# Performance work log

Measured on AMD Instinct MI355X. Metric: run time of the kernel, lower is better.

Reference implementation:

```python
import jax, jax.numpy as jnp
import numpy as np

CLAMP = 80.0


def setup_inputs() -> dict:
    key = jax.random.key(0)
    ks = jax.random.split(key, 8)
    B, C, D, H, W = 2, 64, 16, 16, 16
    Ck = C // 8  # qk channel dim
    x = jax.random.normal(ks[0], (B, C, D, H, W), dtype=jnp.float32)
    # 1x1x1 Conv3d == pointwise linear over channels
    wq = jax.random.normal(ks[1], (Ck, C), dtype=jnp.float32) * (1.0 / np.sqrt(C))
    bq = jnp.zeros((Ck,), dtype=jnp.float32)
    wk = jax.random.normal(ks[2], (Ck, C), dtype=jnp.float32) * (1.0 / np.sqrt(C))
    bk = jnp.zeros((Ck,), dtype=jnp.float32)
    wv = jax.random.normal(ks[3], (C, C), dtype=jnp.float32) * (1.0 / np.sqrt(C))
    bv = jnp.zeros((C,), dtype=jnp.float32)
    gamma = jnp.zeros((1,), dtype=jnp.float32)
    return {"x": x, "wq": wq, "bq": bq, "wk": wk, "bk": bk,
            "wv": wv, "bv": bv, "gamma": gamma}


def reference(x, wq, bq, wk, bk, wv, bv, gamma):
    B, C, D, H, W = x.shape
    N = D * H * W
    scale = 1.0 / np.sqrt(max(C // 8, 1))
    xf = x.reshape(B, C, N)
    # 1x1 convs as channel matmuls -> [B, Cq, N] / [B, C, N]
    q = jnp.einsum('oc,bcn->bon', wq, xf) + bq[None, :, None]
    k = jnp.einsum('oc,bcn->bon', wk, xf) + bk[None, :, None]
    v = jnp.einsum('oc,bcn->bon', wv, xf) + bv[None, :, None]
    q32, k32, v32 = q.astype(jnp.float32), k.astype(jnp.float32), v.astype(jnp.float32)
    # logits[b,n,m] = sum_o q[b,o,n] k[b,o,m] * scale  (q^T k)
    logits = jnp.einsum('bon,bom->bnm', q32, k32) * scale
    logits = jnp.clip(logits, -CLAMP, CLAMP)
    attn = jax.nn.softmax(logits, axis=-1)  # rows sum to 1
    # out = v @ attn  (note: attn applied on the right, as in source)
    out32 = jnp.einsum('bcn,bnm->bcm', v32, attn)
    out = out32.reshape(B, C, D, H, W).astype(x.dtype)
    return gamma[0] * out + x
```

## Files before the change

kernel.cpp:

```cpp
#include <hip/hip_runtime.h>

#define S2F (0.35355339059327373f * 1.4426950408889634f)

using h2 = decltype(__builtin_amdgcn_cvt_pkrtz(0.0f, 0.0f));
typedef _Float16 half8 __attribute__((ext_vector_type(8)));
typedef float f32x4 __attribute__((ext_vector_type(4)));

static __device__ __forceinline__ h2 u2h(unsigned u) { return __builtin_bit_cast(h2, u); }
static __device__ __forceinline__ unsigned pkf16(float a, float b) {
  return __builtin_bit_cast(unsigned, __builtin_amdgcn_cvt_pkrtz(a, b));
}
static __device__ __forceinline__ half8 u4h8(uint4 u) { return __builtin_bit_cast(half8, u); }


__global__ void __launch_bounds__(256, 4)
qkv_kernel(const float* __restrict__ x,
           const float* __restrict__ wq, const float* __restrict__ bq,
           const float* __restrict__ wk, const float* __restrict__ bk,
           const float* __restrict__ wv, const float* __restrict__ bv,
           unsigned* __restrict__ q4, unsigned* __restrict__ k4,
           unsigned* __restrict__ v16) {
  __shared__ float wls[16][64];
  __shared__ float bias16[16];
  __shared__ float qk_lds[16][32];
  int t = threadIdx.x;
  int bid = blockIdx.x;
  int b = bid / 640;
  int rem = bid - b * 640;
  int tile = rem / 5;
  int type = rem - tile * 5;
  int n0 = tile << 5;
  int j = t & 31, rg = t >> 5;

  float* wflat = &wls[0][0];
  for (int i = t; i < 1024; i += 256) {
    float wv_;
    if (type == 0) wv_ = (i < 512) ? wq[i] : wk[i - 512];
    else           wv_ = wv[((type - 1) << 10) + i];
    wflat[i] = wv_;
  }
  if (t < 16)
    bias16[t] = (type == 0) ? ((t < 8) ? bq[t] : bk[t - 8])
                            : bv[((type - 1) << 4) + t];
  __syncthreads();

  float res0 = bias16[rg * 2], res1 = bias16[rg * 2 + 1];
  const float* xb = x + ((b * 64) << 12) + n0 + j;
  #pragma unroll 1
  for (int c0 = 0; c0 < 64; c0 += 16) {
    float xr[16];
    #pragma unroll
    for (int cc = 0; cc < 16; ++cc) xr[cc] = xb[(c0 + cc) << 12];
    const float4* w0 = (const float4*)&wls[rg * 2][c0];
    const float4* w1 = (const float4*)&wls[rg * 2 + 1][c0];
    #pragma unroll
    for (int c4 = 0; c4 < 4; ++c4) {
      float4 a = w0[c4], bb = w1[c4];
      res0 += a.x * xr[4*c4] + a.y * xr[4*c4+1] + a.z * xr[4*c4+2] + a.w * xr[4*c4+3];
      res1 += bb.x * xr[4*c4] + bb.y * xr[4*c4+1] + bb.z * xr[4*c4+2] + bb.w * xr[4*c4+3];
    }
  }

  if (type == 0) {
    qk_lds[rg * 2][j] = res0;
    qk_lds[rg * 2 + 1][j] = res1;
    __syncthreads();
    if (t < 64) {
      int jj = t & 31;
      bool isq = t < 32;
      int rb = isq ? 0 : 8;
      float sc = isq ? S2F : 1.0f;
      uint4 u;
      u.x = pkf16(sc * qk_lds[rb + 0][jj], sc * qk_lds[rb + 1][jj]);
      u.y = pkf16(sc * qk_lds[rb + 2][jj], sc * qk_lds[rb + 3][jj]);
      u.z = pkf16(sc * qk_lds[rb + 4][jj], sc * qk_lds[rb + 5][jj]);
      u.w = pkf16(sc * qk_lds[rb + 6][jj], sc * qk_lds[rb + 7][jj]);
      unsigned* dst = isq ? q4 : k4;
      *(uint4*)&dst[((b << 12) + n0 + jj) << 2] = u;
    }
  } else {
    int cbase = (type - 1) << 4;
    unsigned nb0 = (unsigned)__builtin_amdgcn_ds_swizzle(
        __builtin_bit_cast(int, res0), 0x041F);
    unsigned nb1 = (unsigned)__builtin_amdgcn_ds_swizzle(
        __builtin_bit_cast(int, res1), 0x041F);
    if (!(j & 1)) {
      int half = (n0 >> 1) + (j >> 1);
      v16[(((b << 6) + cbase + rg * 2) << 11) + half]     = pkf16(res0, __builtin_bit_cast(float, nb0));
      v16[(((b << 6) + cbase + rg * 2 + 1) << 11) + half] = pkf16(res1, __builtin_bit_cast(float, nb1));
    }
  }
}

__global__ void __launch_bounds__(256, 4)
rowsum_kernel(const unsigned* __restrict__ q4, const unsigned* __restrict__ k4,
              float* __restrict__ lsv2) {
  __shared__ float ps[8][33];
  int t = threadIdx.x;
  int b = blockIdx.x >> 9;
  int nt0 = (blockIdx.x & 511) << 3;
  int tn = t & 7, tg = t >> 3;
  uint4 qu = *(const uint4*)&q4[((b << 12) + nt0 + tn) << 2];
  h2 q0 = u2h(qu.x), q1 = u2h(qu.y), q2 = u2h(qu.z), q3 = u2h(qu.w);
  float acc = 0.f;
  int m0 = tg << 7;
  #pragma unroll 4
  for (int m = m0; m < m0 + 128; ++m) {
    uint4 ka = *(const uint4*)&k4[((b << 12) + m) << 2];
    float l = __builtin_amdgcn_fdot2(u2h(ka.x), q0, 0.f, false);
    l = __builtin_amdgcn_fdot2(u2h(ka.y), q1, l, false);
    l = __builtin_amdgcn_fdot2(u2h(ka.z), q2, l, false);
    l = __builtin_amdgcn_fdot2(u2h(ka.w), q3, l, false);
    acc += exp2f(l);
  }
  ps[tn][tg] = acc;
  __syncthreads();
  if (t < 8) {
    float s = 0.f;
    #pragma unroll
    for (int j = 0; j < 32; ++j) s += ps[t][j];
    lsv2[(b << 12) + nt0 + t] = -__log2f(s);
  }
}

__global__ void __launch_bounds__(512, 1)
attnout_kernel(const float* __restrict__ x, const unsigned* __restrict__ q4,
               const unsigned* __restrict__ k4, const unsigned* __restrict__ v16,
               const float* __restrict__ lsv2, const float* __restrict__ gamma,
               float* __restrict__ out) {
  __shared__ float red[8][64][36];
  int t = threadIdx.x;
  int b = blockIdx.x >> 7;
  int m0 = (blockIdx.x & 127) << 5;
  int w = t >> 6, l = t & 63;
  int L15 = l & 15, G = l >> 4;
  int permG = ((G & 1) << 1) | (G >> 1);
  bool even = (G & 1) == 0;

  uint4 bk2[2];
  #pragma unroll
  for (int mh = 0; mh < 2; ++mh) {
    if (l < 16) bk2[mh] = *(const uint4*)&k4[((b << 12) + m0 + mh * 16 + L15) << 2];
    else        bk2[mh] = make_uint4(0, 0, 0, 0);
  }
  f32x4 acc[2][4];
  #pragma unroll
  for (int mh = 0; mh < 2; ++mh)
    #pragma unroll
    for (int cf = 0; cf < 4; ++cf) acc[mh][cf] = (f32x4){0.f, 0.f, 0.f, 0.f};

  const float* svb = lsv2 + (b << 12);
  const unsigned* q4b = q4 + ((long)(b << 12) << 2);
  const unsigned* v16b = v16 + ((long)(b << 6) << 11);

  auto LOAD = [&](int step, half8& aq0, half8& aq1, f32x4& sv0, f32x4& sv1,
                  uint4* va) {
    int n0 = (w << 9) + (step << 5);
    aq0 = u4h8(*(const uint4*)&q4b[(n0 + L15) << 2]);
    aq1 = u4h8(*(const uint4*)&q4b[(n0 + 16 + L15) << 2]);
    sv0 = *(const f32x4*)&svb[n0 + (G << 2)];
    sv1 = *(const f32x4*)&svb[n0 + 16 + (G << 2)];
    #pragma unroll
    for (int cf = 0; cf < 4; ++cf)
      va[cf] = *(const uint4*)&v16b[(((cf << 4) + L15) << 11) + (n0 >> 1) + (permG << 2)];
  };
  auto COMPUTE = [&](half8 aq0, half8 aq1, f32x4 sv0, f32x4 sv1, const uint4* va) {
    #pragma unroll
    for (int mh = 0; mh < 2; ++mh) {
      f32x4 z = {0.f, 0.f, 0.f, 0.f};
      f32x4 d0 = __builtin_amdgcn_mfma_f32_16x16x32_f16(aq0, u4h8(bk2[mh]), z, 0, 0, 0);
      f32x4 d1 = __builtin_amdgcn_mfma_f32_16x16x32_f16(aq1, u4h8(bk2[mh]), z, 0, 0, 0);
      float p0[4], p1[4];
      #pragma unroll
      for (int r = 0; r < 4; ++r) {
        p0[r] = exp2f(d0[r] + sv0[r]);
        p1[r] = exp2f(d1[r] + sv1[r]);
      }
      unsigned x0 = pkf16(p0[0], p0[1]), x1 = pkf16(p0[2], p0[3]);
      unsigned y0 = pkf16(p1[0], p1[1]), y1 = pkf16(p1[2], p1[3]);
      unsigned snd0 = even ? y0 : x0;
      unsigned snd1 = even ? y1 : x1;
      unsigned r0 = (unsigned)__builtin_amdgcn_ds_swizzle((int)snd0, 0x401F);
      unsigned r1 = (unsigned)__builtin_amdgcn_ds_swizzle((int)snd1, 0x401F);
      uint4 Bu;
      Bu.x = even ? x0 : r0;
      Bu.y = even ? x1 : r1;
      Bu.z = even ? r0 : y0;
      Bu.w = even ? r1 : y1;
      half8 Bf = u4h8(Bu);
      #pragma unroll
      for (int cf = 0; cf < 4; ++cf)
        acc[mh][cf] = __builtin_amdgcn_mfma_f32_16x16x32_f16(u4h8(va[cf]), Bf, acc[mh][cf], 0, 0, 0);
    }
  };

  half8 aq0A, aq1A, aq0B, aq1B;
  f32x4 sv0A, sv1A, sv0B, sv1B;
  uint4 vaA[4], vaB[4];
  LOAD(0, aq0A, aq1A, sv0A, sv1A, vaA);
  #pragma unroll 1
  for (int step = 0; step < 16; step += 2) {
    LOAD(step + 1, aq0B, aq1B, sv0B, sv1B, vaB);
    COMPUTE(aq0A, aq1A, sv0A, sv1A, vaA);
    if (step < 14) LOAD(step + 2, aq0A, aq1A, sv0A, sv1A, vaA);
    COMPUTE(aq0B, aq1B, sv0B, sv1B, vaB);
  }

  #pragma unroll
  for (int mh = 0; mh < 2; ++mh)
    #pragma unroll
    for (int cf = 0; cf < 4; ++cf)
      *(f32x4*)&red[w][l][(mh * 4 + cf) * 4] = acc[mh][cf];
  __syncthreads();
  int rl = t & 63, f = t >> 6;
  float g = gamma[0];
  f32x4 s = {0.f, 0.f, 0.f, 0.f};
  #pragma unroll
  for (int ww = 0; ww < 8; ++ww) s += *(const f32x4*)&red[ww][rl][f * 4];
  int mh = f >> 2, cf = f & 3;
  int m = m0 + mh * 16 + (rl & 15);
  int cb = cf * 16 + ((rl >> 4) << 2);
  #pragma unroll
  for (int r = 0; r < 4; ++r) {
    int idx = (((b << 6) + cb + r) << 12) + m;
    out[idx] = g * s[r] + x[idx];
  }
}

extern "C" void kernel_launch(void* const* d_in, const int* in_sizes, int n_in,
                              void* d_out, int out_size, void* d_ws, size_t ws_size,
                              hipStream_t stream) {
  const float* x     = (const float*)d_in[0];
  const float* wq    = (const float*)d_in[1];
  const float* bq    = (const float*)d_in[2];
  const float* wk    = (const float*)d_in[3];
  const float* bk    = (const float*)d_in[4];
  const float* wv    = (const float*)d_in[5];
  const float* bv    = (const float*)d_in[6];
  const float* gamma = (const float*)d_in[7];
  float* out = (float*)d_out;
  unsigned* wsu = (unsigned*)d_ws;
  unsigned* q4  = wsu;
  unsigned* k4  = wsu + 32768;
  unsigned* v16 = wsu + 65536;
  float*    lsv2 = (float*)(wsu + 327680);

  qkv_kernel<<<1280, 256, 0, stream>>>(x, wq, bq, wk, bk, wv, bv, q4, k4, v16);
  rowsum_kernel<<<1024, 256, 0, stream>>>(q4, k4, lsv2);
  attnout_kernel<<<256, 512, 0, stream>>>(x, q4, k4, v16, lsv2, gamma, out);
}
```

Baseline: 49.75 us.

## Double attnout block to 16 waves splitting the key-row range across more warps

Raises attnout_kernel from 8 to 16 waves per block so each wave handles 256 instead of 512 of the n positions, doubling per-CU latency hiding for the MFMA/exp loop. Q and log-sum values are now loaded inside compute instead of being double-buffered, to save registers. The cross-wave reduction becomes two-stage (upper waves write, lower waves add), and the final write is split so each thread stores two rows. This adds an extra barrier and LDS pass, and 1024-thread blocks with a register cap could cause spills.

```diff
diff --git a/kernel.cpp b/kernel.cpp
--- a/kernel.cpp
+++ b/kernel.cpp
@@ -123,7 +123,7 @@
   }
 }
 
-__global__ void __launch_bounds__(512, 1)
+__global__ void __launch_bounds__(1024, 1)
 attnout_kernel(const float* __restrict__ x, const unsigned* __restrict__ q4,
                const unsigned* __restrict__ k4, const unsigned* __restrict__ v16,
                const float* __restrict__ lsv2, const float* __restrict__ gamma,
@@ -153,18 +153,18 @@
   const unsigned* q4b = q4 + ((long)(b << 12) << 2);
   const unsigned* v16b = v16 + ((long)(b << 6) << 11);
 
-  auto LOAD = [&](int step, half8& aq0, half8& aq1, f32x4& sv0, f32x4& sv1,
-                  uint4* va) {
-    int n0 = (w << 9) + (step << 5);
-    aq0 = u4h8(*(const uint4*)&q4b[(n0 + L15) << 2]);
-    aq1 = u4h8(*(const uint4*)&q4b[(n0 + 16 + L15) << 2]);
-    sv0 = *(const f32x4*)&svb[n0 + (G << 2)];
-    sv1 = *(const f32x4*)&svb[n0 + 16 + (G << 2)];
+  auto LOADVA = [&](int step, uint4* va) {
+    int n0 = (w << 8) + (step << 5);
     #pragma unroll
     for (int cf = 0; cf < 4; ++cf)
       va[cf] = *(const uint4*)&v16b[(((cf << 4) + L15) << 11) + (n0 >> 1) + (permG << 2)];
   };
-  auto COMPUTE = [&](half8 aq0, half8 aq1, f32x4 sv0, f32x4 sv1, const uint4* va) {
+  auto COMPUTE = [&](int step, const uint4* va) {
+    int n0 = (w << 8) + (step << 5);
+    half8 aq0 = u4h8(*(const uint4*)&q4b[(n0 + L15) << 2]);
+    half8 aq1 = u4h8(*(const uint4*)&q4b[(n0 + 16 + L15) << 2]);
+    f32x4 sv0 = *(const f32x4*)&svb[n0 + (G << 2)];
+    f32x4 sv1 = *(const f32x4*)&svb[n0 + 16 + (G << 2)];
     #pragma unroll
     for (int mh = 0; mh < 2; ++mh) {
       f32x4 z = {0.f, 0.f, 0.f, 0.f};
@@ -194,34 +194,48 @@
     }
   };
 
-  half8 aq0A, aq1A, aq0B, aq1B;
-  f32x4 sv0A, sv1A, sv0B, sv1B;
   uint4 vaA[4], vaB[4];
-  LOAD(0, aq0A, aq1A, sv0A, sv1A, vaA);
+  LOADVA(0, vaA);
   #pragma unroll 1
-  for (int step = 0; step < 16; step += 2) {
-    LOAD(step + 1, aq0B, aq1B, sv0B, sv1B, vaB);
-    COMPUTE(aq0A, aq1A, sv0A, sv1A, vaA);
-    if (step < 14) LOAD(step + 2, aq0A, aq1A, sv0A, sv1A, vaA);
-    COMPUTE(aq0B, aq1B, sv0B, sv1B, vaB);
-  }
-
-  #pragma unroll
-  for (int mh = 0; mh < 2; ++mh)
-    #pragma unroll
-    for (int cf = 0; cf < 4; ++cf)
-      *(f32x4*)&red[w][l][(mh * 4 + cf) * 4] = acc[mh][cf];
-  __syncthreads();
-  int rl = t & 63, f = t >> 6;
+  for (int step = 0; step < 8; step += 2) {
+    LOADVA(step + 1, vaB);
+    COMPUTE(step, vaA);
+    if (step < 6) LOADVA(step + 2, vaA);
+    COMPUTE(step + 1, vaB);
+  }
+
+  if (w >= 8) {
+    #pragma unroll
+    for (int mh = 0; mh < 2; ++mh)
+      #pragma unroll
+      for (int cf = 0; cf < 4; ++cf)
+        *(f32x4*)&red[w - 8][l][(mh * 4 + cf) * 4] = acc[mh][cf];
+  }
+  __syncthreads();
+  if (w < 8) {
+    #pragma unroll
+    for (int mh = 0; mh < 2; ++mh)
+      #pragma unroll
+      for (int cf = 0; cf < 4; ++cf) {
+        f32x4 o = *(const f32x4*)&red[w][l][(mh * 4 + cf) * 4];
+        o += acc[mh][cf];
+        *(f32x4*)&red[w][l][(mh * 4 + cf) * 4] = o;
+      }
+  }
+  __syncthreads();
+  int rl = t & 63;
+  int fidx = (t >> 6) & 7;
+  int rh = t >> 9;
   float g = gamma[0];
   f32x4 s = {0.f, 0.f, 0.f, 0.f};
   #pragma unroll
-  for (int ww = 0; ww < 8; ++ww) s += *(const f32x4*)&red[ww][rl][f * 4];
-  int mh = f >> 2, cf = f & 3;
+  for (int ww = 0; ww < 8; ++ww) s += *(const f32x4*)&red[ww][rl][fidx * 4];
+  int mh = fidx >> 2, cf = fidx & 3;
   int m = m0 + mh * 16 + (rl & 15);
   int cb = cf * 16 + ((rl >> 4) << 2);
   #pragma unroll
-  for (int r = 0; r < 4; ++r) {
+  for (int rr = 0; rr < 2; ++rr) {
+    int r = rh * 2 + rr;
     int idx = (((b << 6) + cb + r) << 12) + m;
     out[idx] = g * s[r] + x[idx];
   }
@@ -247,5 +261,5 @@
 
   qkv_kernel<<<1280, 256, 0, stream>>>(x, wq, bq, wk, bk, wv, bv, q4, k4, v16);
   rowsum_kernel<<<1024, 256, 0, stream>>>(q4, k4, lsv2);
-  attnout_kernel<<<256, 512, 0, stream>>>(x, q4, k4, v16, lsv2, gamma, out);
-}
+  attnout_kernel<<<256, 1024, 0, stream>>>(x, q4, k4, v16, lsv2, gamma, out);
+}
```

After: 51.52 us. 3.6% more time.
